# Kernel tuning notes

Hardware: AMD Instinct MI355X
Metric: run time of the kernel (lower is better)

The kernel has to match this reference:

```python
import jax, jax.numpy as jnp
import numpy as np

BS, SEQ, INP, HID = 64, 512, 512, 1024

def setup_inputs() -> dict:
    key = jax.random.key(0)
    k1, k2, k3, k4, k5 = jax.random.split(key, 5)
    scale_ih = 1.0 / np.sqrt(HID)
    return {
        "x_in": jax.random.normal(k1, (BS, SEQ, INP), dtype=jnp.float32),
        "W_ih": jax.random.normal(k2, (HID, INP), dtype=jnp.float32) * scale_ih,
        "W_hh": jax.random.normal(k3, (HID, HID), dtype=jnp.float32) * scale_ih,
        "b_ih": jax.random.normal(k4, (HID,), dtype=jnp.float32) * scale_ih,
        "b_hh": jax.random.normal(k5, (HID,), dtype=jnp.float32) * scale_ih,
    }

def reference(x_in, W_ih, W_hh, b_ih, b_hh):
    # batch_first=True: x_in is (B, S, F); permute to (S, B, F)
    x = jnp.swapaxes(x_in, 0, 1)
    # Precompute input projection for all timesteps in one big GEMM: (S, B, H)
    xw = jnp.einsum('sbf,hf->sbh', x, W_ih) + b_ih + b_hh
    h0 = jnp.zeros((x_in.shape[0], W_hh.shape[0]), dtype=x_in.dtype)

    def step(h, xt):
        # RNNCell: h' = tanh(x W_ih^T + b_ih + h W_hh^T + b_hh)
        h_new = jnp.tanh(xt + h @ W_hh.T)
        return h_new, h_new

    _, hiddens = jax.lax.scan(step, h0, xw)  # (S, B, H)
    return jnp.swapaxes(hiddens, 0, 1)  # back to (B, S, H)
```

## Files before the change

### kernel.cpp

```cpp
#include <hip/hip_runtime.h>

#define BATCH 64
#define SEQ   512
#define INP   512
#define HID   1024
#define MAGIC 0x13570000u

__global__ __launch_bounds__(256) void xw_gemm(
    const float* __restrict__ X, const float* __restrict__ Wih,
    const float* __restrict__ bih, const float* __restrict__ bhh,
    float* __restrict__ out)
{
    __shared__ float As[8][128];
    __shared__ float Bs[8][128];
    const int t  = threadIdx.x;
    const int m0 = blockIdx.x * 128;
    const int n0 = blockIdx.y * 128;
    const int lr = t >> 1;
    const int lk = (t & 1) * 4;
    const int ty = t >> 4;
    const int tx = t & 15;

    float acc[8][8];
#pragma unroll
    for (int i = 0; i < 8; ++i)
#pragma unroll
        for (int j = 0; j < 8; ++j) acc[i][j] = 0.f;

    const float* xrow = X   + (size_t)(m0 + lr) * INP + lk;
    const float* wrow = Wih + (size_t)(n0 + lr) * INP + lk;

    for (int k0 = 0; k0 < INP; k0 += 8) {
        float4 av = *(const float4*)(xrow + k0);
        float4 bv = *(const float4*)(wrow + k0);
        __syncthreads();
        As[lk + 0][lr] = av.x; As[lk + 1][lr] = av.y;
        As[lk + 2][lr] = av.z; As[lk + 3][lr] = av.w;
        Bs[lk + 0][lr] = bv.x; Bs[lk + 1][lr] = bv.y;
        Bs[lk + 2][lr] = bv.z; Bs[lk + 3][lr] = bv.w;
        __syncthreads();
#pragma unroll
        for (int kk = 0; kk < 8; ++kk) {
            float4 a0 = *(const float4*)&As[kk][ty * 4];
            float4 a1 = *(const float4*)&As[kk][64 + ty * 4];
            float4 b0 = *(const float4*)&Bs[kk][tx * 4];
            float4 b1 = *(const float4*)&Bs[kk][64 + tx * 4];
            float am[8] = {a0.x, a0.y, a0.z, a0.w, a1.x, a1.y, a1.z, a1.w};
            float bn[8] = {b0.x, b0.y, b0.z, b0.w, b1.x, b1.y, b1.z, b1.w};
#pragma unroll
            for (int i = 0; i < 8; ++i)
#pragma unroll
                for (int j = 0; j < 8; ++j)
                    acc[i][j] = fmaf(am[i], bn[j], acc[i][j]);
        }
    }

    const int nA = n0 + tx * 4;
    const int nB = n0 + 64 + tx * 4;
    float4 bA1 = *(const float4*)(bih + nA);
    float4 bA2 = *(const float4*)(bhh + nA);
    float4 bB1 = *(const float4*)(bih + nB);
    float4 bB2 = *(const float4*)(bhh + nB);
    float4 biasA = make_float4(bA1.x + bA2.x, bA1.y + bA2.y, bA1.z + bA2.z, bA1.w + bA2.w);
    float4 biasB = make_float4(bB1.x + bB2.x, bB1.y + bB2.y, bB1.z + bB2.z, bB1.w + bB2.w);

#pragma unroll
    for (int i = 0; i < 8; ++i) {
        int mloc = (i < 4) ? (ty * 4 + i) : (64 + ty * 4 + (i - 4));
        size_t m = (size_t)(m0 + mloc);
        float4 vA = make_float4(acc[i][0] + biasA.x, acc[i][1] + biasA.y,
                                acc[i][2] + biasA.z, acc[i][3] + biasA.w);
        float4 vB = make_float4(acc[i][4] + biasB.x, acc[i][5] + biasB.y,
                                acc[i][6] + biasB.z, acc[i][7] + biasB.w);
        *(float4*)(out + m * HID + nA) = vA;
        *(float4*)(out + m * HID + nB) = vB;
    }
}

__global__ __launch_bounds__(256) void rnn_scan(
    const float* __restrict__ Whh, float* __restrict__ out,
    unsigned* __restrict__ flags)
{
    __shared__ float4 Wlds[16][256];

    const int t  = threadIdx.x;
    const int g  = blockIdx.x >> 6;
    const int jt = blockIdx.x & 63;

    {
        const int r  = t >> 4;
        const int cb = t & 15;
        const float4* src = (const float4*)(Whh + (size_t)(jt * 16 + r) * HID);
#pragma unroll
        for (int i = 0; i < 16; ++i) {
            int c4 = i * 16 + cb;
            Wlds[r][(c4 + r) & 255] = src[c4];
        }
    }

    const int lane = t & 63;
    const int wv   = t >> 6;
    const int kc   = lane >> 4;
    const int jl   = lane & 15;
    const int bb   = g * 16 + wv * 4;

    __syncthreads();

    for (int s = 0; s < SEQ; ++s) {
        float a0 = 0.f, a1 = 0.f, a2 = 0.f, a3 = 0.f;

        if (s > 0) {
            if (t < 64) {
                const unsigned want = MAGIC + (unsigned)(s - 1);
                unsigned* f = flags + ((((s - 1) & 7) * 4 + g) * 64 + t);
                while (__hip_atomic_load(f, __ATOMIC_RELAXED, __HIP_MEMORY_SCOPE_AGENT) != want)
                    __builtin_amdgcn_s_sleep(1);
            }
            __syncthreads();
            __builtin_amdgcn_fence(__ATOMIC_ACQUIRE, "agent");

            const float4* h0 = (const float4*)(out + ((size_t)(bb + 0) * SEQ + (s - 1)) * HID);
            const float4* h1 = (const float4*)(out + ((size_t)(bb + 1) * SEQ + (s - 1)) * HID);
            const float4* h2 = (const float4*)(out + ((size_t)(bb + 2) * SEQ + (s - 1)) * HID);
            const float4* h3 = (const float4*)(out + ((size_t)(bb + 3) * SEQ + (s - 1)) * HID);

#pragma unroll 4
            for (int i = 0; i < 64; ++i) {
                const int L = kc * 64 + i;
                const float4 w4 = Wlds[jl][(L + jl) & 255];
                const float4 x0 = h0[L];
                const float4 x1 = h1[L];
                const float4 x2 = h2[L];
                const float4 x3 = h3[L];
                a0 = fmaf(x0.x, w4.x, a0); a0 = fmaf(x0.y, w4.y, a0);
                a0 = fmaf(x0.z, w4.z, a0); a0 = fmaf(x0.w, w4.w, a0);
                a1 = fmaf(x1.x, w4.x, a1); a1 = fmaf(x1.y, w4.y, a1);
                a1 = fmaf(x1.z, w4.z, a1); a1 = fmaf(x1.w, w4.w, a1);
                a2 = fmaf(x2.x, w4.x, a2); a2 = fmaf(x2.y, w4.y, a2);
                a2 = fmaf(x2.z, w4.z, a2); a2 = fmaf(x2.w, w4.w, a2);
                a3 = fmaf(x3.x, w4.x, a3); a3 = fmaf(x3.y, w4.y, a3);
                a3 = fmaf(x3.z, w4.z, a3); a3 = fmaf(x3.w, w4.w, a3);
            }
            a0 += __shfl_xor(a0, 16); a0 += __shfl_xor(a0, 32);
            a1 += __shfl_xor(a1, 16); a1 += __shfl_xor(a1, 32);
            a2 += __shfl_xor(a2, 16); a2 += __shfl_xor(a2, 32);
            a3 += __shfl_xor(a3, 16); a3 += __shfl_xor(a3, 32);
        }

        if (lane < 16) {
            const int j = jt * 16 + jl;
            float* p0 = out + ((size_t)(bb + 0) * SEQ + s) * HID + j;
            float* p1 = out + ((size_t)(bb + 1) * SEQ + s) * HID + j;
            float* p2 = out + ((size_t)(bb + 2) * SEQ + s) * HID + j;
            float* p3 = out + ((size_t)(bb + 3) * SEQ + s) * HID + j;
            float v0 = tanhf(*p0 + a0);
            float v1 = tanhf(*p1 + a1);
            float v2 = tanhf(*p2 + a2);
            float v3 = tanhf(*p3 + a3);
            __hip_atomic_store(p0, v0, __ATOMIC_RELAXED, __HIP_MEMORY_SCOPE_AGENT);
            __hip_atomic_store(p1, v1, __ATOMIC_RELAXED, __HIP_MEMORY_SCOPE_AGENT);
            __hip_atomic_store(p2, v2, __ATOMIC_RELAXED, __HIP_MEMORY_SCOPE_AGENT);
            __hip_atomic_store(p3, v3, __ATOMIC_RELAXED, __HIP_MEMORY_SCOPE_AGENT);
        }
        __syncthreads();
        if (t == 0)
            __hip_atomic_store(flags + (((s & 7) * 4 + g) * 64 + jt),
                               MAGIC + (unsigned)s,
                               __ATOMIC_RELAXED, __HIP_MEMORY_SCOPE_AGENT);
    }
}

extern "C" void kernel_launch(void* const* d_in, const int* in_sizes, int n_in,
                              void* d_out, int out_size, void* d_ws, size_t ws_size,
                              hipStream_t stream)
{
    (void)in_sizes; (void)n_in; (void)out_size; (void)ws_size;
    const float* x   = (const float*)d_in[0];
    const float* Wih = (const float*)d_in[1];
    const float* Whh = (const float*)d_in[2];
    const float* bih = (const float*)d_in[3];
    const float* bhh = (const float*)d_in[4];
    float* out = (float*)d_out;
    unsigned* flags = (unsigned*)d_ws;

    dim3 g1(BATCH * SEQ / 128, HID / 128);
    xw_gemm<<<g1, 256, 0, stream>>>(x, Wih, bih, bhh, out);
    rnn_scan<<<256, 256, 0, stream>>>(Whh, out, flags);
}
```

Measured before the change: 8.904 ms.

## Double the scan block to 512 threads, prefetch h chunks and hoist xw loads

The recurrent scan kernel now runs 512 threads per block, so each wave covers 8 output columns for 4 batch rows and each lane reduces a 32-float4 slice of K. The hidden-state loads are software-pipelined with a register double buffer across 8 chunks, and the precomputed xw value is loaded before the flag wait so its latency sits off the critical path. The aim is to shorten the per-step latency of the serial recurrence through more memory-level parallelism and less work per lane. The cost is higher register pressure from the prefetch buffers and one extra shuffle stage in the reduction.

```diff
diff --git a/kernel.cpp b/kernel.cpp
--- a/kernel.cpp
+++ b/kernel.cpp
@@ -77,7 +77,7 @@
     }
 }
 
-__global__ __launch_bounds__(256) void rnn_scan(
+__global__ __launch_bounds__(512, 2) void rnn_scan(
     const float* __restrict__ Whh, float* __restrict__ out,
     unsigned* __restrict__ flags)
 {
@@ -88,25 +88,37 @@
     const int jt = blockIdx.x & 63;
 
     {
-        const int r  = t >> 4;
-        const int cb = t & 15;
+        const int r  = t >> 5;
+        const int cb = t & 31;
         const float4* src = (const float4*)(Whh + (size_t)(jt * 16 + r) * HID);
 #pragma unroll
-        for (int i = 0; i < 16; ++i) {
-            int c4 = i * 16 + cb;
+        for (int i = 0; i < 8; ++i) {
+            int c4 = i * 32 + cb;
             Wlds[r][(c4 + r) & 255] = src[c4];
         }
     }
 
     const int lane = t & 63;
     const int wv   = t >> 6;
-    const int kc   = lane >> 4;
-    const int jl   = lane & 15;
-    const int bb   = g * 16 + wv * 4;
+    const int wb   = wv >> 1;
+    const int wj   = wv & 1;
+    const int kc   = lane >> 3;
+    const int jl   = lane & 7;
+    const int rw   = wj * 8 + jl;
+    const int bb   = g * 16 + wb * 4;
+    const int j    = jt * 16 + rw;
 
     __syncthreads();
 
     for (int s = 0; s < SEQ; ++s) {
+        float xw0 = 0.f, xw1 = 0.f, xw2 = 0.f, xw3 = 0.f;
+        if (lane < 8) {
+            xw0 = out[((size_t)(bb + 0) * SEQ + s) * HID + j];
+            xw1 = out[((size_t)(bb + 1) * SEQ + s) * HID + j];
+            xw2 = out[((size_t)(bb + 2) * SEQ + s) * HID + j];
+            xw3 = out[((size_t)(bb + 3) * SEQ + s) * HID + j];
+        }
+
         float a0 = 0.f, a1 = 0.f, a2 = 0.f, a3 = 0.f;
 
         if (s > 0) {
@@ -124,39 +136,72 @@
             const float4* h2 = (const float4*)(out + ((size_t)(bb + 2) * SEQ + (s - 1)) * HID);
             const float4* h3 = (const float4*)(out + ((size_t)(bb + 3) * SEQ + (s - 1)) * HID);
 
-#pragma unroll 4
-            for (int i = 0; i < 64; ++i) {
-                const int L = kc * 64 + i;
-                const float4 w4 = Wlds[jl][(L + jl) & 255];
-                const float4 x0 = h0[L];
-                const float4 x1 = h1[L];
-                const float4 x2 = h2[L];
-                const float4 x3 = h3[L];
-                a0 = fmaf(x0.x, w4.x, a0); a0 = fmaf(x0.y, w4.y, a0);
-                a0 = fmaf(x0.z, w4.z, a0); a0 = fmaf(x0.w, w4.w, a0);
-                a1 = fmaf(x1.x, w4.x, a1); a1 = fmaf(x1.y, w4.y, a1);
-                a1 = fmaf(x1.z, w4.z, a1); a1 = fmaf(x1.w, w4.w, a1);
-                a2 = fmaf(x2.x, w4.x, a2); a2 = fmaf(x2.y, w4.y, a2);
-                a2 = fmaf(x2.z, w4.z, a2); a2 = fmaf(x2.w, w4.w, a2);
-                a3 = fmaf(x3.x, w4.x, a3); a3 = fmaf(x3.y, w4.y, a3);
-                a3 = fmaf(x3.z, w4.z, a3); a3 = fmaf(x3.w, w4.w, a3);
+            const int base = kc * 32;
+
+            float4 cur[4][4];
+#pragma unroll
+            for (int i = 0; i < 4; ++i) {
+                cur[i][0] = h0[base + i];
+                cur[i][1] = h1[base + i];
+                cur[i][2] = h2[base + i];
+                cur[i][3] = h3[base + i];
             }
-            a0 += __shfl_xor(a0, 16); a0 += __shfl_xor(a0, 32);
-            a1 += __shfl_xor(a1, 16); a1 += __shfl_xor(a1, 32);
-            a2 += __shfl_xor(a2, 16); a2 += __shfl_xor(a2, 32);
-            a3 += __shfl_xor(a3, 16); a3 += __shfl_xor(a3, 32);
-        }
-
-        if (lane < 16) {
-            const int j = jt * 16 + jl;
+
+#pragma unroll
+            for (int ch = 0; ch < 8; ++ch) {
+                float4 nxt[4][4];
+                if (ch < 7) {
+                    const int nb = base + (ch + 1) * 4;
+#pragma unroll
+                    for (int i = 0; i < 4; ++i) {
+                        nxt[i][0] = h0[nb + i];
+                        nxt[i][1] = h1[nb + i];
+                        nxt[i][2] = h2[nb + i];
+                        nxt[i][3] = h3[nb + i];
+                    }
+                }
+#pragma unroll
+                for (int i = 0; i < 4; ++i) {
+                    const int L = base + ch * 4 + i;
+                    const float4 w4 = Wlds[rw][(L + rw) & 255];
+                    const float4 x0 = cur[i][0];
+                    const float4 x1 = cur[i][1];
+                    const float4 x2 = cur[i][2];
+                    const float4 x3 = cur[i][3];
+                    a0 = fmaf(x0.x, w4.x, a0); a0 = fmaf(x0.y, w4.y, a0);
+                    a0 = fmaf(x0.z, w4.z, a0); a0 = fmaf(x0.w, w4.w, a0);
+                    a1 = fmaf(x1.x, w4.x, a1); a1 = fmaf(x1.y, w4.y, a1);
+                    a1 = fmaf(x1.z, w4.z, a1); a1 = fmaf(x1.w, w4.w, a1);
+                    a2 = fmaf(x2.x, w4.x, a2); a2 = fmaf(x2.y, w4.y, a2);
+                    a2 = fmaf(x2.z, w4.z, a2); a2 = fmaf(x2.w, w4.w, a2);
+                    a3 = fmaf(x3.x, w4.x, a3); a3 = fmaf(x3.y, w4.y, a3);
+                    a3 = fmaf(x3.z, w4.z, a3); a3 = fmaf(x3.w, w4.w, a3);
+                }
+                if (ch < 7) {
+#pragma unroll
+                    for (int i = 0; i < 4; ++i) {
+                        cur[i][0] = nxt[i][0];
+                        cur[i][1] = nxt[i][1];
+                        cur[i][2] = nxt[i][2];
+                        cur[i][3] = nxt[i][3];
+                    }
+                }
+            }
+            a0 += __shfl_xor(a0, 8); a0 += __shfl_xor(a0, 16); a0 += __shfl_xor(a0, 32);
+            a1 += __shfl_xor(a1, 8); a1 += __shfl_xor(a1, 16); a1 += __shfl_xor(a1, 32);
+            a2 += __shfl_xor(a2, 8); a2 += __shfl_xor(a2, 16); a2 += __shfl_xor(a2, 32);
+            a3 += __shfl_xor(a3, 8); a3 += __shfl_xor(a3, 16); a3 += __shfl_xor(a3, 32);
+        }
+
+        if (lane < 8) {
             float* p0 = out + ((size_t)(bb + 0) * SEQ + s) * HID + j;
             float* p1 = out + ((size_t)(bb + 1) * SEQ + s) * HID + j;
             float* p2 = out + ((size_t)(bb + 2) * SEQ + s) * HID + j;
             float* p3 = out + ((size_t)(bb + 3) * SEQ + s) * HID + j;
-            float v0 = tanhf(*p0 + a0);
-            float v1 = tanhf(*p1 + a1);
-            float v2 = tanhf(*p2 + a2);
-            float v3 = tanhf(*p3 + a3);
+            float v0 = tanhf(xw0 + a0);
+            float v1 = tanhf(xw1 + a1);
+            float v2 = tanhf(xw2 + a2);
+            float v3 = tanhf(xw3 + a3);
             __hip_atomic_store(p0, v0, __ATOMIC_RELAXED, __HIP_MEMORY_SCOPE_AGENT);
             __hip_atomic_store(p1, v1, __ATOMIC_RELAXED, __HIP_MEMORY_SCOPE_AGENT);
             __hip_atomic_store(p2, v2, __ATOMIC_RELAXED, __HIP_MEMORY_SCOPE_AGENT);
@@ -185,5 +230,5 @@
 
     dim3 g1(BATCH * SEQ / 128, HID / 128);
     xw_gemm<<<g1, 256, 0, stream>>>(x, Wih, bih, bhh, out);
-    rnn_scan<<<256, 256, 0, stream>>>(Whh, out, flags);
+    rnn_scan<<<256, 512, 0, stream>>>(Whh, out, flags);
 }
```

After: 12.29 ms. 38.0% more time.

## Keep W_hh slice in registers, stage h in LDS, split K across waves

Applied to the files above, without the earlier changes.

The recurrent scan kernel now keeps each thread's slice of W_hh in registers instead of LDS. Each step it stages the previous hidden rows for 8 batches into LDS with coalesced loads. The K dimension is split across the four waves, and partial sums are combined through a small shared buffer before tanh. The grid doubles to 512 persistent blocks in 8 batch groups of 8, with launch bounds requesting 2 blocks per CU. The aim is to cut per-step global h reads and shorten the critical path, at the cost of more blocks taking part in the spin-wait flag synchronisation, which relies on all 512 blocks being co-resident.

```diff
diff --git a/kernel.cpp b/kernel.cpp
--- a/kernel.cpp
+++ b/kernel.cpp
@@ -5,6 +5,11 @@
 #define INP   512
 #define HID   1024
 #define MAGIC 0x13570000u
+
+#define NG 8
+#define GB 8
+#define NJT 64
+#define TJ 16
 
 __global__ __launch_bounds__(256) void xw_gemm(
     const float* __restrict__ X, const float* __restrict__ Wih,
@@ -77,94 +82,107 @@
     }
 }
 
-__global__ __launch_bounds__(256) void rnn_scan(
+__global__ __launch_bounds__(256, 2) void rnn_scan(
     const float* __restrict__ Whh, float* __restrict__ out,
     unsigned* __restrict__ flags)
 {
-    __shared__ float4 Wlds[16][256];
-
-    const int t  = threadIdx.x;
-    const int g  = blockIdx.x >> 6;
-    const int jt = blockIdx.x & 63;
-
+    __shared__ float4 Hlds[GB][256];
+    __shared__ float  Pbuf[4][GB][TJ];
+
+    const int t    = threadIdx.x;
+    const int g    = blockIdx.x >> 6;
+    const int jt   = blockIdx.x & 63;
+    const int lane = t & 63;
+    const int w    = t >> 6;
+    const int kc2  = (lane >> 4) & 3;
+    const int jl   = lane & 15;
+    const int base4 = w * 64 + kc2 * 16;
+
+    float4 Wreg[16];
     {
-        const int r  = t >> 4;
-        const int cb = t & 15;
-        const float4* src = (const float4*)(Whh + (size_t)(jt * 16 + r) * HID);
-#pragma unroll
-        for (int i = 0; i < 16; ++i) {
-            int c4 = i * 16 + cb;
-            Wlds[r][(c4 + r) & 255] = src[c4];
-        }
-    }
-
-    const int lane = t & 63;
-    const int wv   = t >> 6;
-    const int kc   = lane >> 4;
-    const int jl   = lane & 15;
-    const int bb   = g * 16 + wv * 4;
-
-    __syncthreads();
+        const float4* wr = (const float4*)(Whh + (size_t)(jt * TJ + jl) * HID) + base4;
+#pragma unroll
+        for (int q = 0; q < 4; ++q) {
+            const int rot = 4 * ((kc2 + q) & 3);
+#pragma unroll
+            for (int r = 0; r < 4; ++r)
+                Wreg[q * 4 + r] = wr[rot + r];
+        }
+    }
+
+    const int bo = t >> 4;
+    const int jo = t & 15;
 
     for (int s = 0; s < SEQ; ++s) {
-        float a0 = 0.f, a1 = 0.f, a2 = 0.f, a3 = 0.f;
+        float xw = 0.f;
+        if (t < 128)
+            xw = out[((size_t)(g * GB + bo) * SEQ + s) * HID + jt * TJ + jo];
+
+        float p[GB];
+#pragma unroll
+        for (int b = 0; b < GB; ++b) p[b] = 0.f;
 
         if (s > 0) {
             if (t < 64) {
                 const unsigned want = MAGIC + (unsigned)(s - 1);
-                unsigned* f = flags + ((((s - 1) & 7) * 4 + g) * 64 + t);
+                unsigned* f = flags + ((((s - 1) & 3) * NG + g) * 64 + t);
                 while (__hip_atomic_load(f, __ATOMIC_RELAXED, __HIP_MEMORY_SCOPE_AGENT) != want)
                     __builtin_amdgcn_s_sleep(1);
             }
             __syncthreads();
             __builtin_amdgcn_fence(__ATOMIC_ACQUIRE, "agent");
 
-            const float4* h0 = (const float4*)(out + ((size_t)(bb + 0) * SEQ + (s - 1)) * HID);
-            const float4* h1 = (const float4*)(out + ((size_t)(bb + 1) * SEQ + (s - 1)) * HID);
-            const float4* h2 = (const float4*)(out + ((size_t)(bb + 2) * SEQ + (s - 1)) * HID);
-            const float4* h3 = (const float4*)(out + ((size_t)(bb + 3) * SEQ + (s - 1)) * HID);
-
-#pragma unroll 4
-            for (int i = 0; i < 64; ++i) {
-                const int L = kc * 64 + i;
-                const float4 w4 = Wlds[jl][(L + jl) & 255];
-                const float4 x0 = h0[L];
-                const float4 x1 = h1[L];
-                const float4 x2 = h2[L];
-                const float4 x3 = h3[L];
-                a0 = fmaf(x0.x, w4.x, a0); a0 = fmaf(x0.y, w4.y, a0);
-                a0 = fmaf(x0.z, w4.z, a0); a0 = fmaf(x0.w, w4.w, a0);
-                a1 = fmaf(x1.x, w4.x, a1); a1 = fmaf(x1.y, w4.y, a1);
-                a1 = fmaf(x1.z, w4.z, a1); a1 = fmaf(x1.w, w4.w, a1);
-                a2 = fmaf(x2.x, w4.x, a2); a2 = fmaf(x2.y, w4.y, a2);
-                a2 = fmaf(x2.z, w4.z, a2); a2 = fmaf(x2.w, w4.w, a2);
-                a3 = fmaf(x3.x, w4.x, a3); a3 = fmaf(x3.y, w4.y, a3);
-                a3 = fmaf(x3.z, w4.z, a3); a3 = fmaf(x3.w, w4.w, a3);
-            }
-            a0 += __shfl_xor(a0, 16); a0 += __shfl_xor(a0, 32);
-            a1 += __shfl_xor(a1, 16); a1 += __shfl_xor(a1, 32);
-            a2 += __shfl_xor(a2, 16); a2 += __shfl_xor(a2, 32);
-            a3 += __shfl_xor(a3, 16); a3 += __shfl_xor(a3, 32);
+#pragma unroll
+            for (int rr = 0; rr < 2; ++rr) {
+                const int b = w * 2 + rr;
+                const float4* hrow =
+                    (const float4*)(out + ((size_t)(g * GB + b) * SEQ + (s - 1)) * HID);
+#pragma unroll
+                for (int i2 = 0; i2 < 4; ++i2)
+                    Hlds[b][i2 * 64 + lane] = hrow[i2 * 64 + lane];
+            }
+            __syncthreads();
+
+#pragma unroll
+            for (int q = 0; q < 4; ++q) {
+                const int rot = 4 * ((kc2 + q) & 3);
+#pragma unroll
+                for (int r = 0; r < 4; ++r) {
+                    const float4 wv = Wreg[q * 4 + r];
+#pragma unroll
+                    for (int b = 0; b < GB; ++b) {
+                        const float4 h4 = Hlds[b][base4 + rot + r];
+                        p[b] = fmaf(wv.x, h4.x, p[b]);
+                        p[b] = fmaf(wv.y, h4.y, p[b]);
+                        p[b] = fmaf(wv.z, h4.z, p[b]);
+                        p[b] = fmaf(wv.w, h4.w, p[b]);
+                    }
+                }
+            }
+#pragma unroll
+            for (int b = 0; b < GB; ++b) {
+                p[b] += __shfl_xor(p[b], 16);
+                p[b] += __shfl_xor(p[b], 32);
+            }
         }
 
         if (lane < 16) {
-            const int j = jt * 16 + jl;
-            float* p0 = out + ((size_t)(bb + 0) * SEQ + s) * HID + j;
-            float* p1 = out + ((size_t)(bb + 1) * SEQ + s) * HID + j;
-            float* p2 = out + ((size_t)(bb + 2) * SEQ + s) * HID + j;
-            float* p3 = out + ((size_t)(bb + 3) * SEQ + s) * HID + j;
-            float v0 = tanhf(*p0 + a0);
-            float v1 = tanhf(*p1 + a1);
-            float v2 = tanhf(*p2 + a2);
-            float v3 = tanhf(*p3 + a3);
-            __hip_atomic_store(p0, v0, __ATOMIC_RELAXED, __HIP_MEMORY_SCOPE_AGENT);
-            __hip_atomic_store(p1, v1, __ATOMIC_RELAXED, __HIP_MEMORY_SCOPE_AGENT);
-            __hip_atomic_store(p2, v2, __ATOMIC_RELAXED, __HIP_MEMORY_SCOPE_AGENT);
-            __hip_atomic_store(p3, v3, __ATOMIC_RELAXED, __HIP_MEMORY_SCOPE_AGENT);
+#pragma unroll
+            for (int b = 0; b < GB; ++b) Pbuf[w][b][jl] = p[b];
+        }
+        __syncthreads();
+
+        if (t < 128) {
+            float tot = xw + Pbuf[0][bo][jo] + Pbuf[1][bo][jo]
+                           + Pbuf[2][bo][jo] + Pbuf[3][bo][jo];
+            float v = tanhf(tot);
+            __hip_atomic_store(
+                out + ((size_t)(g * GB + bo) * SEQ + s) * HID + jt * TJ + jo,
+                v, __ATOMIC_RELAXED, __HIP_MEMORY_SCOPE_AGENT);
         }
         __syncthreads();
         if (t == 0)
-            __hip_atomic_store(flags + (((s & 7) * 4 + g) * 64 + jt),
+            __hip_atomic_store(flags + (((s & 3) * NG + g) * 64 + jt),
                                MAGIC + (unsigned)s,
                                __ATOMIC_RELAXED, __HIP_MEMORY_SCOPE_AGENT);
     }
@@ -185,5 +203,5 @@
 
     dim3 g1(BATCH * SEQ / 128, HID / 128);
     xw_gemm<<<g1, 256, 0, stream>>>(x, Wih, bih, bhh, out);
-    rnn_scan<<<256, 256, 0, stream>>>(Whh, out, flags);
+    rnn_scan<<<NG * NJT, 256, 0, stream>>>(Whh, out, flags);
 }
```

After: 10.17 ms. 1.14x slower.
